# Kernel tuning notes

Measured on AMD Instinct MI355X. Metric: run time of the kernel, lower is better.

## Reference

```python
import jax, jax.numpy as jnp
import numpy as np

B, S, IN = 8, 512, 128
D, H, DK, DV, DFF, L = 512, 8, 64, 64, 2048, 4
LOCAL = 64
EPS = 1e-5


def setup_inputs() -> dict:
    key = jax.random.key(0)
    ks = jax.random.split(key, 12)
    w = lambda k, shape: (jax.random.normal(k, shape, jnp.float32) * 0.02)
    return dict(
        x=jax.random.normal(ks[0], (B, S, IN), jnp.float32),
        We=w(ks[1], (IN, D)), be=jnp.zeros((D,), jnp.float32),
        Wq=w(ks[2], (L, D, H * DK)), bq=jnp.zeros((L, H * DK), jnp.float32),
        Wk=w(ks[3], (L, D, H * DK)), bk=jnp.zeros((L, H * DK), jnp.float32),
        Wv=w(ks[4], (L, D, H * DV)), bv=jnp.zeros((L, H * DV), jnp.float32),
        Wo=w(ks[5], (L, H * DV, D)), bo=jnp.zeros((L, D), jnp.float32),
        ln1_g=jnp.ones((L, D), jnp.float32), ln1_b=jnp.zeros((L, D), jnp.float32),
        W1=w(ks[6], (L, D, DFF)), b1=jnp.zeros((L, DFF), jnp.float32),
        W2=w(ks[7], (L, DFF, D)), b2=jnp.zeros((L, D), jnp.float32),
        ln2_g=jnp.ones((L, D), jnp.float32), ln2_b=jnp.zeros((L, D), jnp.float32),
    )


def _layernorm(x, g, b):
    m = jnp.mean(x, -1, keepdims=True)
    v = jnp.mean((x - m) ** 2, -1, keepdims=True)
    return (x - m) / jnp.sqrt(v + EPS) * g + b


def _gelu(x):
    # GELU tanh approximation exactly as in the torch module
    return 0.5 * x * (1.0 + jnp.tanh(np.sqrt(2.0 / np.pi) * (x + 0.044715 * x ** 3)))


def _sincos_pe():
    pos = jnp.arange(S, dtype=jnp.float32)[:, None]
    div = jnp.exp(jnp.arange(0, D, 2, dtype=jnp.float32) * (-np.log(10000.0) / D))
    pe = jnp.zeros((S, D), jnp.float32)
    pe = pe.at[:, 0::2].set(jnp.sin(pos * div))
    pe = pe.at[:, 1::2].set(jnp.cos(pos * div))
    return pe


def _forward(x, We, be, Wq, bq, Wk, bk, Wv, bv, Wo, bo,
             ln1_g, ln1_b, W1, b1, W2, b2, ln2_g, ln2_b):
    h = x @ We + be + _sincos_pe()  # [B,S,D]
    idx = jnp.arange(S)
    # local band mask: positions farther than LOCAL are masked with -1e9
    mask = jnp.abs(idx[:, None] - idx[None, :]) > LOCAL  # [S,S] bool

    def mha(hin, l):
        q = (hin @ Wq[l] + bq[l]).reshape(B, S, H, DK).transpose(0, 2, 1, 3)
        k = (hin @ Wk[l] + bk[l]).reshape(B, S, H, DK).transpose(0, 2, 1, 3)
        v = (hin @ Wv[l] + bv[l]).reshape(B, S, H, DV).transpose(0, 2, 1, 3)
        scores = jnp.einsum('bhqd,bhkd->bhqk', q, k) / np.sqrt(DK)
        scores = jnp.where(mask, -1e9, scores)
        a = jax.nn.softmax(scores, axis=-1)
        ctx = jnp.einsum('bhqk,bhkd->bhqd', a, v)
        ctx = ctx.transpose(0, 2, 1, 3).reshape(B, S, H * DV)
        out = ctx @ Wo[l] + bo[l]
        return _layernorm(out + hin, ln1_g[l], ln1_b[l]), a

    attns = []
    for l in range(L):
        h, a = mha(h, l)
        h, a = mha(h, l)  # local=True: second pass with the SAME weights
        ff = _gelu(h @ W1[l] + b1[l]) @ W2[l] + b2[l]
        h = _layernorm(ff + h, ln2_g[l], ln2_b[l])
        attns.append(a)
    attns = jnp.stack(attns).transpose(1, 0, 2, 3, 4)  # [B,L,H,S,S]
    return h, attns


def reference(x, We, be, Wq, bq, Wk, bk, Wv, bv, Wo, bo,
              ln1_g, ln1_b, W1, b1, W2, b2, ln2_g, ln2_b):
    return _forward(x, We, be, Wq, bq, Wk, bk, Wv, bv, Wo, bo,
                    ln1_g, ln1_b, W1, b1, W2, b2, ln2_g, ln2_b)
```

## Files before the change

### kernel.cpp

```cpp
#include <hip/hip_runtime.h>

using bf16 = __bf16;
using bf16x8 = __attribute__((ext_vector_type(8))) __bf16;
using bf16x4 = __attribute__((ext_vector_type(4))) __bf16;
using f32x4  = __attribute__((ext_vector_type(4))) float;

#define AS1(p) ((const __attribute__((address_space(1))) unsigned int*)(p))
#define AS3(p) ((__attribute__((address_space(3))) unsigned int*)(p))

template<int N> __device__ __forceinline__ void wait_vmcnt() {
    if constexpr (N == 0) asm volatile("s_waitcnt vmcnt(0)" ::: "memory");
    else if constexpr (N == 3) asm volatile("s_waitcnt vmcnt(3)" ::: "memory");
    else if constexpr (N == 4) asm volatile("s_waitcnt vmcnt(4)" ::: "memory");
    else if constexpr (N == 6) asm volatile("s_waitcnt vmcnt(6)" ::: "memory");
    else if constexpr (N == 8) asm volatile("s_waitcnt vmcnt(8)" ::: "memory");
}

template<int TM, int EPI>
__global__ __launch_bounds__(256, TM == 64 ? 4 : 3)
void gemm_kernel(const bf16* __restrict__ A, const bf16* __restrict__ WT,
                 const float* __restrict__ bias, bf16* __restrict__ Cbf,
                 float* __restrict__ Cf, const float* __restrict__ PE,
                 int K, int ldc, int gx, int q8)
{
    constexpr int NA  = TM / 16;
    constexpr int NCH = NA + 8;
    constexpr int CPW = NCH / 4;
    constexpr int MI  = TM / 32;
    constexpr int ASZ = TM * 32;
    constexpr int BSZ = 128 * 32;
    __shared__ bf16 Asm[3 * ASZ];
    __shared__ bf16 Bsm[3 * BSZ];
    const int tid = threadIdx.x;
    const int lane = tid & 63;
    const int w  = tid >> 6;
    const int wr = w >> 1, wc = w & 1;
    const int l4 = lane & 15, lg = lane >> 4;

    const int bid = blockIdx.x;
    const int s  = (bid & 7) * q8 + (bid >> 3);
    const int by = s / gx, bx = s - by * gx;
    const size_t m0 = (size_t)by * TM;
    const size_t n0 = (size_t)bx * 128;

    f32x4 acc[MI][4] = {};

    const int lr  = lane >> 2;
    const int ksw = (((lane & 3) ^ ((lane >> 3) & 3)) * 8);
    const bf16* src[CPW];
    bf16* dst0[CPW];
    int step[CPW];
    #pragma unroll
    for (int ci = 0; ci < CPW; ++ci) {
        const int c = w * CPW + ci;
        if (c < NA) {
            src[ci]  = A + (m0 + (size_t)(c * 16 + lr)) * K + ksw;
            dst0[ci] = Asm + c * 512;
            step[ci] = ASZ;
        } else {
            src[ci]  = WT + (n0 + (size_t)((c - NA) * 16 + lr)) * K + ksw;
            dst0[ci] = Bsm + (c - NA) * 512;
            step[ci] = BSZ;
        }
    }
    const int rsw = (lg ^ ((l4 >> 1) & 3)) * 8;
    const bf16* Ar = &Asm[(wr * (TM / 2) + l4) * 32 + rsw];
    const bf16* Br = &Bsm[(wc * 64 + l4) * 32 + rsw];

    auto STAGE = [&](int b) {
        #pragma unroll
        for (int ci = 0; ci < CPW; ++ci) {
            __builtin_amdgcn_global_load_lds(AS1(src[ci]),
                                             AS3(dst0[ci] + b * step[ci]), 16, 0, 0);
            src[ci] += 32;
        }
    };

    const int nt = K >> 5;
    STAGE(0);
    if (nt > 1) STAGE(1);

    int cur = 0;
    for (int t = 0; t < nt; ++t) {
        if (t + 2 < nt) {
            int pb = cur - 1; if (pb < 0) pb = 2;
            STAGE(pb);
            wait_vmcnt<2 * CPW>();
        } else if (t + 1 < nt) {
            wait_vmcnt<CPW>();
        } else {
            wait_vmcnt<0>();
        }
        __builtin_amdgcn_s_barrier();
        const bf16* Ac = Ar + cur * ASZ;
        const bf16* Bc = Br + cur * BSZ;
        bf16x8 aF[MI], bF[4];
        #pragma unroll
        for (int i = 0; i < MI; ++i) aF[i] = *(const bf16x8*)(Ac + i * 512);
        #pragma unroll
        for (int i = 0; i < 4; ++i) bF[i] = *(const bf16x8*)(Bc + i * 512);
        #pragma unroll
        for (int mi = 0; mi < MI; ++mi)
            #pragma unroll
            for (int ni = 0; ni < 4; ++ni)
                acc[mi][ni] = __builtin_amdgcn_mfma_f32_16x16x32_bf16(
                    aF[mi], bF[ni], acc[mi][ni], 0, 0, 0);
        asm volatile("s_waitcnt lgkmcnt(0)" ::: "memory");
        __builtin_amdgcn_s_barrier();
        cur = (cur == 2) ? 0 : cur + 1;
    }

    #pragma unroll
    for (int ni = 0; ni < 4; ++ni) {
        const int col = (int)n0 + wc * 64 + ni * 16 + l4;
        const float bv = bias[col];
        #pragma unroll
        for (int mi = 0; mi < MI; ++mi) {
            const int row0 = (int)m0 + wr * (TM / 2) + mi * 16 + lg * 4;
            #pragma unroll
            for (int r = 0; r < 4; ++r) {
                float v = acc[mi][ni][r] + bv;
                const int row = row0 + r;
                if (EPI == 1) {
                    float u = 1.5957691216057308f * (v + 0.044715f * v * v * v);
                    v = v / (1.0f + __expf(-u));
                }
                if (EPI == 2) {
                    v += PE[((row & 511) << 9) + col];
                    Cf[(size_t)row * ldc + col] = v;
                }
                Cbf[(size_t)row * ldc + col] = (bf16)v;
            }
        }
    }
}

template<int WRITE_ATTN>
__global__ __launch_bounds__(256, 2)
void attn_kernel(const bf16* __restrict__ qkv, bf16* __restrict__ ctx,
                 float* __restrict__ attn_out )
{
    __shared__ bf16 Ks[192 * 72];
    __shared__ bf16 Vt[64 * 200];
    __shared__ bf16 Ps[64 * 200];
    const int tid = threadIdx.x;
    const int lane = tid & 63, w = tid >> 6;
    const int l4 = lane & 15, lg = lane >> 4;
    const int bh = blockIdx.y, ib = blockIdx.x;
    const int b = bh >> 3, hd = bh & 7;
    const int i0 = ib * 64;
    const int j0 = (i0 >= 64) ? i0 - 64 : 0;
    const int j1 = (i0 + 128 <= 512) ? i0 + 128 : 512;
    const int W = j1 - j0;
    const size_t rowb = (size_t)b * 512;

    if (WRITE_ATTN) {
        float* arow = attn_out + (size_t)b * 8388608 + (size_t)hd * 262144 +
                      (size_t)i0 * 512;
        const int zr = tid >> 2, p = tid & 3;
        f32x4 z = {0.f, 0.f, 0.f, 0.f};
        f32x4* rp = (f32x4*)(arow + (size_t)zr * 512);
        for (int c = p; c < (j0 >> 2); c += 4) rp[c] = z;
        for (int c = (j1 >> 2) + p; c < 128; c += 4) rp[c] = z;
    }

    for (int it = 0; it < 6; ++it) {
        int chunk = tid + it * 256;
        int j = chunk >> 3, k0 = (chunk & 7) * 8;
        if (j < W) {
            bf16x8 v = *(const bf16x8*)(qkv + (rowb + j0 + j) * 1536 + 512 + hd * 64 + k0);
            *(bf16x8*)(&Ks[j * 72 + k0]) = v;
        }
    }
    for (int it = 0; it < 6; ++it) {
        int chunk = tid + it * 256;
        int j = chunk >> 3, d0 = (chunk & 7) * 8;
        if (j < W) {
            bf16x8 v = *(const bf16x8*)(qkv + (rowb + j0 + j) * 1536 + 1024 + hd * 64 + d0);
            #pragma unroll
            for (int e = 0; e < 8; ++e) Vt[(d0 + e) * 200 + j] = v[e];
        }
    }
    bf16x8 qF0, qF1;
    {
        const bf16* qrow = qkv + (rowb + i0 + w * 16 + l4) * 1536 + hd * 64;
        qF0 = *(const bf16x8*)(qrow + lg * 8);
        qF1 = *(const bf16x8*)(qrow + 32 + lg * 8);
    }
    __syncthreads();

    f32x4 s[12];
    #pragma unroll
    for (int t = 0; t < 12; ++t) s[t] = (f32x4){0.f, 0.f, 0.f, 0.f};
    const int NT = W >> 4;
    for (int t = 0; t < NT; ++t) {
        const bf16* kb = &Ks[(t * 16 + l4) * 72];
        bf16x8 b0 = *(const bf16x8*)(kb + lg * 8);
        bf16x8 b1 = *(const bf16x8*)(kb + 32 + lg * 8);
        s[t] = __builtin_amdgcn_mfma_f32_16x16x32_bf16(qF0, b0, s[t], 0, 0, 0);
        s[t] = __builtin_amdgcn_mfma_f32_16x16x32_bf16(qF1, b1, s[t], 0, 0, 0);
    }
    const int irow0 = i0 + w * 16 + lg * 4;
    float pm[4] = {-3e38f, -3e38f, -3e38f, -3e38f};
    for (int t = 0; t < NT; ++t) {
        int jg = j0 + t * 16 + l4;
        #pragma unroll
        for (int r = 0; r < 4; ++r) {
            int dd = irow0 + r - jg;
            float sv = s[t][r] * 0.125f;
            if (dd > 64 || dd < -64) sv = -1e30f;
            s[t][r] = sv;
            pm[r] = fmaxf(pm[r], sv);
        }
    }
    #pragma unroll
    for (int d = 1; d < 16; d <<= 1)
        #pragma unroll
        for (int r = 0; r < 4; ++r) pm[r] = fmaxf(pm[r], __shfl_xor(pm[r], d));
    float ps[4] = {0.f, 0.f, 0.f, 0.f};
    for (int t = 0; t < NT; ++t)
        #pragma unroll
        for (int r = 0; r < 4; ++r) {
            float p = __expf(s[t][r] - pm[r]);
            s[t][r] = p;
            ps[r] += p;
        }
    #pragma unroll
    for (int d = 1; d < 16; d <<= 1)
        #pragma unroll
        for (int r = 0; r < 4; ++r) ps[r] += __shfl_xor(ps[r], d);
    float rinv[4];
    #pragma unroll
    for (int r = 0; r < 4; ++r) rinv[r] = 1.0f / ps[r];

    for (int t = 0; t < NT; ++t) {
        #pragma unroll
        for (int r = 0; r < 4; ++r) {
            float p = s[t][r] * rinv[r];
            Ps[(w * 16 + lg * 4 + r) * 200 + t * 16 + l4] = (bf16)p;
            if (WRITE_ATTN) {
                size_t off = (size_t)b * 8388608 + (size_t)hd * 262144 +
                             (size_t)(i0 + w * 16 + lg * 4 + r) * 512 +
                             (size_t)(j0 + t * 16 + l4);
                attn_out[off] = p;
            }
        }
    }
    f32x4 o[4] = {};
    const int KS = W >> 5;
    for (int ks = 0; ks < KS; ++ks) {
        bf16x8 aF = *(const bf16x8*)(&Ps[(w * 16 + l4) * 200 + ks * 32 + lg * 8]);
        #pragma unroll
        for (int ni = 0; ni < 4; ++ni) {
            bf16x8 bF = *(const bf16x8*)(&Vt[(ni * 16 + l4) * 200 + ks * 32 + lg * 8]);
            o[ni] = __builtin_amdgcn_mfma_f32_16x16x32_bf16(aF, bF, o[ni], 0, 0, 0);
        }
    }
    #pragma unroll
    for (int ni = 0; ni < 4; ++ni)
        #pragma unroll
        for (int r = 0; r < 4; ++r)
            ctx[(rowb + i0 + w * 16 + lg * 4 + r) * 512 + hd * 64 + ni * 16 + l4] =
                (bf16)o[ni][r];
}

__global__ __launch_bounds__(256)
void ln_kernel(const bf16* __restrict__ y, const float* hin,
               const float* __restrict__ g, const float* __restrict__ bb,
               float* hf, bf16* __restrict__ hbf)
{
    const int row = blockIdx.x * 4 + (threadIdx.x >> 6);
    const int lane = threadIdx.x & 63;
    const size_t base = (size_t)row * 512 + lane * 8;
    bf16x8 yv = *(const bf16x8*)(y + base);
    f32x4 h0 = *(const f32x4*)(hin + base);
    f32x4 h1 = *(const f32x4*)(hin + base + 4);
    float x[8];
    #pragma unroll
    for (int i = 0; i < 8; ++i) x[i] = (float)yv[i] + (i < 4 ? h0[i] : h1[i - 4]);
    float s = 0.f, q = 0.f;
    #pragma unroll
    for (int i = 0; i < 8; ++i) { s += x[i]; q += x[i] * x[i]; }
    #pragma unroll
    for (int d = 1; d < 64; d <<= 1) { s += __shfl_xor(s, d); q += __shfl_xor(q, d); }
    const float m = s * 0.001953125f;
    const float var = q * 0.001953125f - m * m;
    const float rstd = rsqrtf(var + 1e-5f);
    const int c0 = lane * 8;
    f32x4 g0 = *(const f32x4*)(g + c0), g1v = *(const f32x4*)(g + c0 + 4);
    f32x4 b0 = *(const f32x4*)(bb + c0), b1v = *(const f32x4*)(bb + c0 + 4);
    f32x4 o0, o1;
    bf16x8 ob;
    #pragma unroll
    for (int i = 0; i < 8; ++i) {
        float gg = i < 4 ? g0[i] : g1v[i - 4];
        float bv = i < 4 ? b0[i] : b1v[i - 4];
        float o = (x[i] - m) * rstd * gg + bv;
        if (i < 4) o0[i] = o; else o1[i - 4] = o;
        ob[i] = (bf16)o;
    }
    *(f32x4*)(hf + base) = o0;
    *(f32x4*)(hf + base + 4) = o1;
    *(bf16x8*)(hbf + base) = ob;
}

struct TMat { const float* src; size_t dst; int K; int N; int tile0; };
struct TDesc { TMat m[26]; };

__global__ __launch_bounds__(256)
void wtrans_kernel(TDesc d, bf16* __restrict__ wbuf)
{
    __shared__ float tile[32][33];
    int t = blockIdx.x;
    int mi = 0;
    while (t >= d.m[mi + 1].tile0) ++mi;
    const TMat mm = d.m[mi];
    const int lt = t - mm.tile0;
    const int tpr = mm.N >> 5;
    const int kt = lt / tpr, nt = lt % tpr;
    const int r = threadIdx.x >> 5, c = threadIdx.x & 31;
    #pragma unroll
    for (int it = 0; it < 4; ++it)
        tile[r + it * 8][c] =
            mm.src[(size_t)(kt * 32 + r + it * 8) * mm.N + nt * 32 + c];
    __syncthreads();
    #pragma unroll
    for (int it = 0; it < 4; ++it)
        wbuf[mm.dst + (size_t)(nt * 32 + r + it * 8) * mm.K + kt * 32 + c] =
            (bf16)tile[c][r + it * 8];
}

__global__ void prep_kernel(const float* __restrict__ x, bf16* __restrict__ xbf,
                            float* __restrict__ pe,
                            const float* bq, const float* bk, const float* bv,
                            float* __restrict__ bqkv)
{
    const int bid = blockIdx.x;
    if (bid < 512) {
        int i = bid * 256 + threadIdx.x;
        f32x4 v = *(const f32x4*)(x + (size_t)i * 4);
        bf16x4 o;
        #pragma unroll
        for (int e = 0; e < 4; ++e) o[e] = (bf16)v[e];
        *(bf16x4*)(xbf + (size_t)i * 4) = o;
    } else if (bid < 1024) {
        int i = (bid - 512) * 256 + threadIdx.x;
        int s = i >> 8, d2 = i & 255;
        float ang = (float)s * expf((float)(2 * d2) * -0.017988946039016f);
        pe[(s << 9) + 2 * d2]     = sinf(ang);
        pe[(s << 9) + 2 * d2 + 1] = cosf(ang);
    } else {
        int i = (bid - 1024) * 256 + threadIdx.x;
        if (i < 6144) {
            int l = i / 1536, c = i - l * 1536;
            float v;
            if (c < 512) v = bq[l * 512 + c];
            else if (c < 1024) v = bk[l * 512 + c - 512];
            else v = bv[l * 512 + c - 1024];
            bqkv[i] = v;
        }
    }
}

extern "C" void kernel_launch(void* const* d_in, const int* in_sizes, int n_in,
                              void* d_out, int out_size, void* d_ws, size_t ws_size,
                              hipStream_t stream)
{
    const float* x   = (const float*)d_in[0];
    const float* We  = (const float*)d_in[1];
    const float* be  = (const float*)d_in[2];
    const float* Wq  = (const float*)d_in[3];
    const float* bq  = (const float*)d_in[4];
    const float* Wk  = (const float*)d_in[5];
    const float* bk  = (const float*)d_in[6];
    const float* Wv  = (const float*)d_in[7];
    const float* bv  = (const float*)d_in[8];
    const float* Wo  = (const float*)d_in[9];
    const float* bo  = (const float*)d_in[10];
    const float* g1  = (const float*)d_in[11];
    const float* b1n = (const float*)d_in[12];
    const float* W1  = (const float*)d_in[13];
    const float* b1f = (const float*)d_in[14];
    const float* W2  = (const float*)d_in[15];
    const float* b2f = (const float*)d_in[16];
    const float* g2  = (const float*)d_in[17];
    const float* b2n = (const float*)d_in[18];

    char* ws = (char*)d_ws;
    bf16* wbuf = (bf16*)ws;
    size_t off = 12648448ull * 2;
    float* bqkv = (float*)(ws + off); off += 6144ull * 4;
    float* pe   = (float*)(ws + off); off += 262144ull * 4;
    bf16* xbf   = (bf16*)(ws + off);  off += 524288ull * 2;
    float* h    = (float*)(ws + off); off += 2097152ull * 4;
    bf16* hbf   = (bf16*)(ws + off);  off += 2097152ull * 2;
    bf16* qkvb  = (bf16*)(ws + off);  off += 6291456ull * 2;
    bf16* ctx   = (bf16*)(ws + off);  off += 2097152ull * 2;
    bf16* tmp   = (bf16*)(ws + off);  off += 2097152ull * 2;
    bf16* ffn   = (bf16*)(ws + off);  off += 8388608ull * 2;
    (void)ws_size; (void)in_sizes; (void)n_in; (void)out_size;

    float* out_h = (float*)d_out;
    float* out_attn = out_h + 2097152;

    TDesc td{};
    int tile = 0, e = 0;
    auto add = [&](const float* src, size_t dst, int K, int N) {
        td.m[e].src = src; td.m[e].dst = dst; td.m[e].K = K; td.m[e].N = N;
        td.m[e].tile0 = tile; tile += (K >> 5) * (N >> 5); ++e;
    };
    add(We, 0, 128, 512);
    for (int l = 0; l < 4; ++l) {
        size_t base = 65536 + (size_t)l * 3145728;
        add(Wq + (size_t)l * 262144,  base + 0,       512, 512);
        add(Wk + (size_t)l * 262144,  base + 262144,  512, 512);
        add(Wv + (size_t)l * 262144,  base + 524288,  512, 512);
        add(Wo + (size_t)l * 262144,  base + 786432,  512, 512);
        add(W1 + (size_t)l * 1048576, base + 1048576, 512, 2048);
        add(W2 + (size_t)l * 1048576, base + 2097152, 2048, 512);
    }
    td.m[e].tile0 = tile;

    wtrans_kernel<<<dim3(tile), dim3(256), 0, stream>>>(td, wbuf);
    prep_kernel<<<dim3(1048), dim3(256), 0, stream>>>(x, xbf, pe, bq, bk, bv, bqkv);

    gemm_kernel<64, 2><<<dim3(256), dim3(256), 0, stream>>>(
        xbf, wbuf, be, hbf, h, pe, 128, 512, 4, 32);

    for (int l = 0; l < 4; ++l) {
        const bf16* WqkvT = wbuf + 65536 + (size_t)l * 3145728;
        const bf16* WoT   = WqkvT + 786432;
        const bf16* W1T   = WqkvT + 1048576;
        const bf16* W2T   = WqkvT + 2097152;
        for (int pass = 0; pass < 2; ++pass) {
            gemm_kernel<128, 0><<<dim3(384), dim3(256), 0, stream>>>(
                hbf, WqkvT, bqkv + l * 1536, qkvb, (float*)nullptr, (float*)nullptr,
                512, 1536, 12, 48);
            if (pass == 0)
                attn_kernel<0><<<dim3(8, 64), dim3(256), 0, stream>>>(
                    qkvb, ctx, (float*)nullptr);
            else
                attn_kernel<1><<<dim3(8, 64), dim3(256), 0, stream>>>(
                    qkvb, ctx, out_attn + (size_t)l * 2097152);
            gemm_kernel<64, 0><<<dim3(256), dim3(256), 0, stream>>>(
                ctx, WoT, bo + l * 512, tmp, (float*)nullptr, (float*)nullptr,
                512, 512, 4, 32);
            ln_kernel<<<dim3(1024), dim3(256), 0, stream>>>(
                tmp, h, g1 + l * 512, b1n + l * 512, h, hbf);
        }
        gemm_kernel<128, 1><<<dim3(512), dim3(256), 0, stream>>>(
            hbf, W1T, b1f + l * 2048, ffn, (float*)nullptr, (float*)nullptr,
            512, 2048, 16, 64);
        gemm_kernel<64, 0><<<dim3(256), dim3(256), 0, stream>>>(
            ffn, W2T, b2f + l * 512, tmp, (float*)nullptr, (float*)nullptr,
            2048, 512, 4, 32);
        float* hout = (l == 3) ? out_h : h;
        ln_kernel<<<dim3(1024), dim3(256), 0, stream>>>(
            tmp, h, g2 + l * 512, b2n + l * 512, hout, hbf);
    }
}
```

Measured before the change: 702.4 us.

## Stage GEMM and attention outputs through LDS for vectorized stores, alias attention LDS

For the non-PE GEMM epilogues, results are written into a padded shared-memory tile and then stored to global memory as 16-byte vectors, replacing scattered 2-byte stores. The attention kernel does the same for its context output, reusing the V buffer as staging. It also aliases the K and P shared buffers to cut LDS use so three blocks can share a CU, and raises wave priority around the MFMA loops. The cost is extra barriers and LDS round trips, plus a dependence on correct synchronization between the aliased buffers.

After: 714.9 us. No clear change (+1.8%).

```diff
diff --git a/kernel.cpp b/kernel.cpp
--- a/kernel.cpp
+++ b/kernel.cpp
@@ -29,8 +29,12 @@
     constexpr int MI  = TM / 32;
     constexpr int ASZ = TM * 32;
     constexpr int BSZ = 128 * 32;
-    __shared__ bf16 Asm[3 * ASZ];
-    __shared__ bf16 Bsm[3 * BSZ];
+    constexpr int KELE = 3 * (ASZ + BSZ);
+    constexpr int CELE = TM * 136;
+    constexpr int SMEME = (CELE > KELE) ? CELE : KELE;
+    __shared__ bf16 smem[SMEME];
+    bf16* Asm = smem;
+    bf16* Bsm = smem + 3 * ASZ;
     const int tid = threadIdx.x;
     const int lane = tid & 63;
     const int w  = tid >> 6;
@@ -110,39 +114,64 @@
         cur = (cur == 2) ? 0 : cur + 1;
     }
 
-    #pragma unroll
-    for (int ni = 0; ni < 4; ++ni) {
-        const int col = (int)n0 + wc * 64 + ni * 16 + l4;
-        const float bv = bias[col];
-        #pragma unroll
-        for (int mi = 0; mi < MI; ++mi) {
-            const int row0 = (int)m0 + wr * (TM / 2) + mi * 16 + lg * 4;
+    if (EPI == 2) {
+        #pragma unroll
+        for (int ni = 0; ni < 4; ++ni) {
+            const int col = (int)n0 + wc * 64 + ni * 16 + l4;
+            const float bv = bias[col];
             #pragma unroll
-            for (int r = 0; r < 4; ++r) {
-                float v = acc[mi][ni][r] + bv;
-                const int row = row0 + r;
-                if (EPI == 1) {
-                    float u = 1.5957691216057308f * (v + 0.044715f * v * v * v);
-                    v = v / (1.0f + __expf(-u));
-                }
-                if (EPI == 2) {
+            for (int mi = 0; mi < MI; ++mi) {
+                const int row0 = (int)m0 + wr * (TM / 2) + mi * 16 + lg * 4;
+                #pragma unroll
+                for (int r = 0; r < 4; ++r) {
+                    float v = acc[mi][ni][r] + bv;
+                    const int row = row0 + r;
                     v += PE[((row & 511) << 9) + col];
                     Cf[(size_t)row * ldc + col] = v;
+                    Cbf[(size_t)row * ldc + col] = (bf16)v;
                 }
-                Cbf[(size_t)row * ldc + col] = (bf16)v;
             }
         }
+    } else {
+        bf16* Csm = smem;
+        #pragma unroll
+        for (int ni = 0; ni < 4; ++ni) {
+            const int colL = wc * 64 + ni * 16 + l4;
+            const float bv = bias[(int)n0 + colL];
+            #pragma unroll
+            for (int mi = 0; mi < MI; ++mi) {
+                const int rowL0 = wr * (TM / 2) + mi * 16 + lg * 4;
+                #pragma unroll
+                for (int r = 0; r < 4; ++r) {
+                    float v = acc[mi][ni][r] + bv;
+                    if (EPI == 1) {
+                        float u = 1.5957691216057308f * (v + 0.044715f * v * v * v);
+                        v = v / (1.0f + __expf(-u));
+                    }
+                    Csm[(rowL0 + r) * 136 + colL] = (bf16)v;
+                }
+            }
+        }
+        __syncthreads();
+        #pragma unroll
+        for (int it = 0; it < TM / 16; ++it) {
+            int chunk = tid + it * 256;
+            int rl = chunk >> 4, c0 = (chunk & 15) << 3;
+            *(bf16x8*)(&Cbf[(m0 + rl) * (size_t)ldc + n0 + c0]) =
+                *(const bf16x8*)(&Csm[rl * 136 + c0]);
+        }
     }
 }
 
 template<int WRITE_ATTN>
-__global__ __launch_bounds__(256, 2)
+__global__ __launch_bounds__(256, 3)
 void attn_kernel(const bf16* __restrict__ qkv, bf16* __restrict__ ctx,
                  float* __restrict__ attn_out )
 {
-    __shared__ bf16 Ks[192 * 72];
+    __shared__ bf16 KPs[192 * 72];
     __shared__ bf16 Vt[64 * 200];
-    __shared__ bf16 Ps[64 * 200];
+    bf16* Ks = KPs;
+    bf16* Ps = KPs;
     const int tid = threadIdx.x;
     const int lane = tid & 63, w = tid >> 6;
     const int l4 = lane & 15, lg = lane >> 4;
@@ -193,6 +222,7 @@
     #pragma unroll
     for (int t = 0; t < 12; ++t) s[t] = (f32x4){0.f, 0.f, 0.f, 0.f};
     const int NT = W >> 4;
+    __builtin_amdgcn_s_setprio(1);
     for (int t = 0; t < NT; ++t) {
         const bf16* kb = &Ks[(t * 16 + l4) * 72];
         bf16x8 b0 = *(const bf16x8*)(kb + lg * 8);
@@ -200,6 +230,7 @@
         s[t] = __builtin_amdgcn_mfma_f32_16x16x32_bf16(qF0, b0, s[t], 0, 0, 0);
         s[t] = __builtin_amdgcn_mfma_f32_16x16x32_bf16(qF1, b1, s[t], 0, 0, 0);
     }
+    __builtin_amdgcn_s_setprio(0);
     const int irow0 = i0 + w * 16 + lg * 4;
     float pm[4] = {-3e38f, -3e38f, -3e38f, -3e38f};
     for (int t = 0; t < NT; ++t) {
@@ -232,6 +263,8 @@
     float rinv[4];
     #pragma unroll
     for (int r = 0; r < 4; ++r) rinv[r] = 1.0f / ps[r];
+
+    __syncthreads();
 
     for (int t = 0; t < NT; ++t) {
         #pragma unroll
@@ -248,6 +281,7 @@
     }
     f32x4 o[4] = {};
     const int KS = W >> 5;
+    __builtin_amdgcn_s_setprio(1);
     for (int ks = 0; ks < KS; ++ks) {
         bf16x8 aF = *(const bf16x8*)(&Ps[(w * 16 + l4) * 200 + ks * 32 + lg * 8]);
         #pragma unroll
@@ -256,12 +290,22 @@
             o[ni] = __builtin_amdgcn_mfma_f32_16x16x32_bf16(aF, bF, o[ni], 0, 0, 0);
         }
     }
+    __builtin_amdgcn_s_setprio(0);
+    __syncthreads();
+    bf16* Cs = Vt;
     #pragma unroll
     for (int ni = 0; ni < 4; ++ni)
         #pragma unroll
         for (int r = 0; r < 4; ++r)
-            ctx[(rowb + i0 + w * 16 + lg * 4 + r) * 512 + hd * 64 + ni * 16 + l4] =
-                (bf16)o[ni][r];
+            Cs[(w * 16 + lg * 4 + r) * 64 + ni * 16 + l4] = (bf16)o[ni][r];
+    __syncthreads();
+    #pragma unroll
+    for (int it = 0; it < 2; ++it) {
+        int chunk = tid + it * 256;
+        int rl = chunk >> 3, c0 = (chunk & 7) << 3;
+        *(bf16x8*)(&ctx[(rowb + i0 + rl) * 512 + hd * 64 + c0]) =
+            *(const bf16x8*)(&Cs[rl * 64 + c0]);
+    }
 }
 
 __global__ __launch_bounds__(256)
```
